# Performance work log

Measured on AMD Instinct MI355X. Metric: run time of the kernel, lower is better.

The kernel has to match this reference:

```python
import jax, jax.numpy as jnp
import numpy as np

ALPHA, BETA, DELTA, TAU, GAMMA = 5.0, 0.6, 0.6, 0.5, 0.5
WINDOW, MOMENTUM = 5, 0.999


def setup_inputs() -> dict:
    key = jax.random.key(0)
    k1, k2 = jax.random.split(key)
    B, C, H, W = 32, 256, 64, 64
    F = jax.random.normal(k1, (B, C, H, W), dtype=jnp.float32)
    S = jnp.eye(C, dtype=jnp.float32)          # EMA similarity buffer (initialized as identity)
    U = jax.random.uniform(k2, (B, C), dtype=jnp.float32)  # replaces torch.bernoulli draw
    return {"F": F, "S": S, "U": U}


def _avg_pool(x, win):
    p = win // 2
    s = jax.lax.reduce_window(x, 0.0, jax.lax.add,
                              (1, 1, win, win), (1, 1, 1, 1),
                              [(0, 0), (0, 0), (p, p), (p, p)])
    return s / (win * win)


def _lrd_mask(F, U):
    # Local Response Density sampling -> boolean mask M [B, C]
    B, C, H, W = F.shape
    a = jax.nn.sigmoid(F.mean(axis=(2, 3)))                     # [B, C]
    max_vals = F.reshape(B, C, -1).max(axis=-1)[:, :, None, None]
    M_bin = (F >= DELTA * max_vals).astype(F.dtype)             # [B, C, H, W]
    density = _avg_pool(M_bin, WINDOW)
    d = (density >= TAU).astype(F.dtype).mean(axis=(2, 3))      # [B, C]
    s = a ** GAMMA * d ** (1.0 - GAMMA)
    s_max = s.max(axis=1, keepdims=True)
    prob = jax.nn.sigmoid(ALPHA * (s - BETA * s_max))
    return U < prob                                             # deterministic bernoulli


def _build_perm(m, S):
    # m: [C] bool selected mask, S: [C, C] similarity -> permutation [C] int32
    C = S.shape[0]
    idx = jnp.arange(C)
    unsel = ~m
    # for each channel, most-similar unselected channel (first max, like torch.argmax)
    masked = jnp.where(unsel[None, :], S, -jnp.inf)
    j = jnp.argmax(masked, axis=1)                              # [C]
    perm = jnp.where(m, j, idx)                                 # perm[selected] = j
    targets = jnp.where(m, j, C)                                # C is out-of-range -> dropped
    perm = perm.at[targets].set(idx, mode='drop')               # perm[j] = selected
    valid = m.any() & unsel.any()
    return jnp.where(valid, perm, idx)


def reference(F, S, U):
    B, C, H, W = F.shape
    # EMA update of channel similarity buffer (no_grad in original)
    F_flat = F.reshape(B, C, -1)
    F_norm = F_flat / (jnp.linalg.norm(F_flat, axis=2, keepdims=True) + 1e-6)
    S_batch = jnp.einsum('bcn,bdn->bcd', F_norm, F_norm).mean(axis=0)
    S_new = jax.lax.stop_gradient(MOMENTUM * S + (1.0 - MOMENTUM) * S_batch)
    # LRD sampling mask and per-sample channel-swap permutation
    M = _lrd_mask(jax.lax.stop_gradient(F), U)                  # [B, C] bool
    perm = jax.vmap(_build_perm, in_axes=(0, None))(M, S_new)   # [B, C]
    # structure-aware channel exchange (gather along channel dim)
    gidx = jnp.broadcast_to(perm[:, :, None, None], (B, C, H, W))
    return jnp.take_along_axis(F, gidx, axis=1)
```

## Files before the change

### kernel.cpp

```cpp
#include <hip/hip_runtime.h>
#include <math.h>

#define BB 32
#define CC 256
#define HH 64
#define WW 64
#define NN 4096

__inline__ __device__ float waveReduceSum(float v) {
    #pragma unroll
    for (int off = 32; off > 0; off >>= 1) v += __shfl_xor(v, off);
    return v;
}
__inline__ __device__ float waveReduceMax(float v) {
    #pragma unroll
    for (int off = 32; off > 0; off >>= 1) v = fmaxf(v, __shfl_xor(v, off));
    return v;
}

__global__ __launch_bounds__(256) void k_prep(const float* __restrict__ F,
                                              float* __restrict__ inv_norm,
                                              float* __restrict__ s_score) {
    const int plane = blockIdx.x;
    const int tid = threadIdx.x;
    __shared__ float bin[4096];
    __shared__ float rowsum[4096];
    __shared__ float swS[4], swQ[4], swM[4];

    const float4* src = (const float4*)(F + (size_t)plane * NN);
    float4 v[4];
    float sum = 0.f, ssq = 0.f, mx = -INFINITY;
    #pragma unroll
    for (int q = 0; q < 4; ++q) {
        v[q] = src[tid + q * 256];
        sum += v[q].x + v[q].y + v[q].z + v[q].w;
        ssq += v[q].x * v[q].x + v[q].y * v[q].y + v[q].z * v[q].z + v[q].w * v[q].w;
        mx = fmaxf(mx, fmaxf(fmaxf(v[q].x, v[q].y), fmaxf(v[q].z, v[q].w)));
    }
    sum = waveReduceSum(sum);
    ssq = waveReduceSum(ssq);
    mx  = waveReduceMax(mx);
    const int w = tid >> 6, ln = tid & 63;
    if (ln == 0) { swS[w] = sum; swQ[w] = ssq; swM[w] = mx; }
    __syncthreads();
    if (tid == 0) {
        swS[0] = swS[0] + swS[1] + swS[2] + swS[3];
        swQ[0] = swQ[0] + swQ[1] + swQ[2] + swQ[3];
        swM[0] = fmaxf(fmaxf(swM[0], swM[1]), fmaxf(swM[2], swM[3]));
    }
    __syncthreads();
    const float totsum = swS[0];
    const float totssq = swQ[0];
    const float thr = 0.6f * swM[0];

    #pragma unroll
    for (int q = 0; q < 4; ++q) {
        const int base = (tid + q * 256) * 4;
        bin[base + 0] = (v[q].x >= thr) ? 1.f : 0.f;
        bin[base + 1] = (v[q].y >= thr) ? 1.f : 0.f;
        bin[base + 2] = (v[q].z >= thr) ? 1.f : 0.f;
        bin[base + 3] = (v[q].w >= thr) ? 1.f : 0.f;
    }
    __syncthreads();

    #pragma unroll
    for (int q = 0; q < 16; ++q) {
        const int p = tid + q * 256;
        const int h = p >> 6, x = p & 63;
        float s5 = 0.f;
        #pragma unroll
        for (int dw = -2; dw <= 2; ++dw) {
            const int xx = x + dw;
            if (xx >= 0 && xx < 64) s5 += bin[h * 64 + xx];
        }
        rowsum[p] = s5;
    }
    __syncthreads();

    int cge = 0;
    #pragma unroll
    for (int q = 0; q < 16; ++q) {
        const int p = tid + q * 256;
        const int h = p >> 6, x = p & 63;
        float cnt = 0.f;
        #pragma unroll
        for (int dh = -2; dh <= 2; ++dh) {
            const int hh = h + dh;
            if (hh >= 0 && hh < 64) cnt += rowsum[hh * 64 + x];
        }
        if (cnt >= 12.5f) cge++;
    }
    float cf = waveReduceSum((float)cge);
    __syncthreads();
    if (ln == 0) swS[w] = cf;
    __syncthreads();
    if (tid == 0) {
        const float total = swS[0] + swS[1] + swS[2] + swS[3];
        const float d = total / 4096.f;
        const float a = 1.f / (1.f + expf(-(totsum / 4096.f)));
        s_score[plane] = sqrtf(a) * sqrtf(d);
        inv_norm[plane] = 1.f / (sqrtf(totssq) + 1e-6f);
    }
}

__global__ __launch_bounds__(256) void k_gram(const float* __restrict__ F,
                                              const float* __restrict__ inv_norm,
                                              float* __restrict__ S_part,
                                              int csh) {
    static const int TI[10] = {0,0,0,0,1,1,1,2,2,3};
    static const int TJ[10] = {0,1,2,3,1,2,3,2,3,3};
    const int t  = blockIdx.x;
    const int bc = blockIdx.y;
    const int b = bc >> csh, chunk = bc & ((1 << csh) - 1);
    const int ti = TI[t], tj = TJ[t];
    const int k0 = chunk << (12 - csh);
    const int iters = 128 >> csh;

    __shared__ float As[32][68];
    __shared__ float Bs[32][68];

    const int tid = threadIdx.x;
    const int lrow = tid >> 2;
    const int kgrp = tid & 3;
    const float* Fb = F + (size_t)b * CC * NN;
    const float scaleA = inv_norm[b * CC + ti * 64 + lrow];
    const float scaleB = inv_norm[b * CC + tj * 64 + lrow];
    const float* gA = Fb + (size_t)(ti * 64 + lrow) * NN + k0 + kgrp * 8;
    const float* gB = Fb + (size_t)(tj * 64 + lrow) * NN + k0 + kgrp * 8;

    const int r0 = (tid >> 4) << 2;
    const int c0 = (tid & 15) << 2;

    float accL2[16];
    #pragma unroll
    for (int e = 0; e < 16; ++e) accL2[e] = 0.f;

    for (int s = 0; s < iters; ++s) {
        const float4 a0 = *(const float4*)(gA);
        const float4 a1 = *(const float4*)(gA + 4);
        const float4 b0 = *(const float4*)(gB);
        const float4 b1 = *(const float4*)(gB + 4);
        __syncthreads();
        const int kb = kgrp * 8;
        As[kb + 0][lrow] = a0.x * scaleA; As[kb + 1][lrow] = a0.y * scaleA;
        As[kb + 2][lrow] = a0.z * scaleA; As[kb + 3][lrow] = a0.w * scaleA;
        As[kb + 4][lrow] = a1.x * scaleA; As[kb + 5][lrow] = a1.y * scaleA;
        As[kb + 6][lrow] = a1.z * scaleA; As[kb + 7][lrow] = a1.w * scaleA;
        Bs[kb + 0][lrow] = b0.x * scaleB; Bs[kb + 1][lrow] = b0.y * scaleB;
        Bs[kb + 2][lrow] = b0.z * scaleB; Bs[kb + 3][lrow] = b0.w * scaleB;
        Bs[kb + 4][lrow] = b1.x * scaleB; Bs[kb + 5][lrow] = b1.y * scaleB;
        Bs[kb + 6][lrow] = b1.z * scaleB; Bs[kb + 7][lrow] = b1.w * scaleB;
        __syncthreads();

        float accL1[16];
        #pragma unroll
        for (int e = 0; e < 16; ++e) accL1[e] = 0.f;
        #pragma unroll
        for (int kk = 0; kk < 32; ++kk) {
            const float4 av = *(const float4*)&As[kk][r0];
            const float4 bv = *(const float4*)&Bs[kk][c0];
            const float ar[4] = {av.x, av.y, av.z, av.w};
            const float br[4] = {bv.x, bv.y, bv.z, bv.w};
            #pragma unroll
            for (int rr = 0; rr < 4; ++rr)
                #pragma unroll
                for (int cc = 0; cc < 4; ++cc)
                    accL1[rr * 4 + cc] += ar[rr] * br[cc];
        }
        #pragma unroll
        for (int e = 0; e < 16; ++e) accL2[e] += accL1[e];
        gA += 32; gB += 32;
    }

    float* dst = S_part + (size_t)(bc * 10 + t) * 4096;
    #pragma unroll
    for (int rr = 0; rr < 4; ++rr)
        #pragma unroll
        for (int cc = 0; cc < 4; ++cc)
            dst[(r0 + rr) * 64 + (c0 + cc)] = accL2[rr * 4 + cc];
}

__global__ __launch_bounds__(256) void k_snew(const float* __restrict__ S_part,
                                              const float* __restrict__ S_old,
                                              float* __restrict__ S_new,
                                              int npart) {
    const int c = blockIdx.x;
    const int d = threadIdx.x;
    if (d < c) return;
    static const int tmap[16] = {0,1,2,3, -1,4,5,6, -1,-1,7,8, -1,-1,-1,9};
    const int t = tmap[((c >> 6) << 2) | (d >> 6)];
    const int r = c & 63, col = d & 63;
    const float* base = S_part + (size_t)t * 4096 + r * 64 + col;
    double sum = 0.0;
    for (int p = 0; p < npart; ++p) sum += (double)base[(size_t)p * 40960];
    const float sb = (float)(sum * (1.0 / 32.0));
    S_new[c * 256 + d] = 0.999f * S_old[c * 256 + d] + 0.001f * sb;
    if (d != c)
        S_new[d * 256 + c] = 0.999f * S_old[d * 256 + c] + 0.001f * sb;
}

__global__ __launch_bounds__(256) void k_perm(const float* __restrict__ s_score,
                                              const float* __restrict__ U,
                                              const float* __restrict__ S_new,
                                              int* __restrict__ perm_g) {
    const int b = blockIdx.x;
    const int c = threadIdx.x;
    __shared__ float red[256];
    __shared__ int m[256];
    __shared__ int jj[256];
    __shared__ int perm[256];

    const float s = s_score[b * 256 + c];
    red[c] = s; __syncthreads();
    for (int off = 128; off > 0; off >>= 1) {
        if (c < off) red[c] = fmaxf(red[c], red[c + off]);
        __syncthreads();
    }
    const float smax = red[0];
    __syncthreads();

    const float prob = 1.f / (1.f + expf(-5.f * (s - 0.6f * smax)));
    const int mi = (U[b * 256 + c] < prob) ? 1 : 0;
    m[c] = mi;
    red[c] = (float)mi;
    __syncthreads();
    for (int off = 128; off > 0; off >>= 1) {
        if (c < off) red[c] += red[c + off];
        __syncthreads();
    }
    const int cnt = (int)red[0];

    float best = -INFINITY; int bj = 0;
    const float* row = S_new + c * 256;
    for (int d2 = 0; d2 < 256; ++d2) {
        const float v = row[d2];
        if (!m[d2] && v > best) { best = v; bj = d2; }
    }
    jj[c] = bj;
    perm[c] = mi ? bj : c;
    __syncthreads();

    const int valid = (cnt > 0) && (cnt < 256);
    if (c == 0 && valid) {
        for (int q = 0; q < 256; ++q)
            if (m[q]) perm[jj[q]] = q;
    }
    __syncthreads();
    perm_g[b * 256 + c] = valid ? perm[c] : c;
}

__global__ __launch_bounds__(256) void k_gather(const float* __restrict__ F,
                                                const int* __restrict__ perm_g,
                                                float* __restrict__ out) {
    const int plane = blockIdx.x;
    const int b = plane >> 8;
    const int p = perm_g[plane];
    const float4* src = (const float4*)(F + ((size_t)b * 256 + p) * NN);
    float4* dst = (float4*)(out + (size_t)plane * NN);
    const int tid = threadIdx.x;
    #pragma unroll
    for (int q = 0; q < 4; ++q) dst[tid + q * 256] = src[tid + q * 256];
}

extern "C" void kernel_launch(void* const* d_in, const int* in_sizes, int n_in,
                              void* d_out, int out_size, void* d_ws, size_t ws_size,
                              hipStream_t stream) {
    const float* F = (const float*)d_in[0];
    const float* S = (const float*)d_in[1];
    const float* U = (const float*)d_in[2];
    float* out = (float*)d_out;

    const size_t need4 = (size_t)128 * 10 * 4096 * 4 + (3 * 8192 + 65536) * 4 + (1 << 16);
    const int csh = (ws_size >= need4) ? 2 : 1;
    const int nch = 1 << csh;
    const int npart = 32 * nch;

    char* ws = (char*)d_ws;
    size_t off = 0;
    float* S_part  = (float*)(ws + off); off += (size_t)npart * 10 * 4096 * 4;
    float* inv_nrm = (float*)(ws + off); off += 8192 * 4;
    float* s_score = (float*)(ws + off); off += 8192 * 4;
    float* S_new   = (float*)(ws + off); off += 65536 * 4;
    int*   perm    = (int*)  (ws + off); off += 8192 * 4;

    k_prep  <<<8192, 256, 0, stream>>>(F, inv_nrm, s_score);
    k_gram  <<<dim3(10, npart), 256, 0, stream>>>(F, inv_nrm, S_part, csh);
    k_snew  <<<256, 256, 0, stream>>>(S_part, S, S_new, npart);
    k_perm  <<<32, 256, 0, stream>>>(s_score, U, S_new, perm);
    k_gather<<<8192, 256, 0, stream>>>(F, perm, out);
}
```

Baseline: 489.2 us.

## Use ballot-based density counting, swizzled gram tiles, and more K-split partitions

The prep kernel now keeps the raw plane in shared memory and computes the 5x5 threshold density with wave ballots and popcounts over bitmasks, replacing the two float shared-memory passes. The gram kernel drops per-element normalization on the shared-memory stores and applies inv_norm at the end. It also XOR-style offsets columns to reduce LDS bank conflicts, uses fmaf accumulation directly, and can split K into 8 chunks when the workspace allows. The EMA reduction uses two accumulators to add ILP. The extra K split raises partial-buffer traffic and reduction work in k_snew.

```diff
diff --git a/kernel.cpp b/kernel.cpp
--- a/kernel.cpp
+++ b/kernel.cpp
@@ -23,8 +23,7 @@
                                               float* __restrict__ s_score) {
     const int plane = blockIdx.x;
     const int tid = threadIdx.x;
-    __shared__ float bin[4096];
-    __shared__ float rowsum[4096];
+    __shared__ float fpl[4096];
     __shared__ float swS[4], swQ[4], swM[4];
 
     const float4* src = (const float4*)(F + (size_t)plane * NN);
@@ -33,6 +32,7 @@
     #pragma unroll
     for (int q = 0; q < 4; ++q) {
         v[q] = src[tid + q * 256];
+        *(float4*)&fpl[(tid + q * 256) * 4] = v[q];
         sum += v[q].x + v[q].y + v[q].z + v[q].w;
         ssq += v[q].x * v[q].x + v[q].y * v[q].y + v[q].z * v[q].z + v[q].w * v[q].w;
         mx = fmaxf(mx, fmaxf(fmaxf(v[q].x, v[q].y), fmaxf(v[q].z, v[q].w)));
@@ -40,8 +40,8 @@
     sum = waveReduceSum(sum);
     ssq = waveReduceSum(ssq);
     mx  = waveReduceMax(mx);
-    const int w = tid >> 6, ln = tid & 63;
-    if (ln == 0) { swS[w] = sum; swQ[w] = ssq; swM[w] = mx; }
+    const int w = tid >> 6, lane = tid & 63;
+    if (lane == 0) { swS[w] = sum; swQ[w] = ssq; swM[w] = mx; }
     __syncthreads();
     if (tid == 0) {
         swS[0] = swS[0] + swS[1] + swS[2] + swS[3];
@@ -52,47 +52,28 @@
     const float totsum = swS[0];
     const float totssq = swQ[0];
     const float thr = 0.6f * swM[0];
-
-    #pragma unroll
-    for (int q = 0; q < 4; ++q) {
-        const int base = (tid + q * 256) * 4;
-        bin[base + 0] = (v[q].x >= thr) ? 1.f : 0.f;
-        bin[base + 1] = (v[q].y >= thr) ? 1.f : 0.f;
-        bin[base + 2] = (v[q].z >= thr) ? 1.f : 0.f;
-        bin[base + 3] = (v[q].w >= thr) ? 1.f : 0.f;
-    }
-    __syncthreads();
-
-    #pragma unroll
-    for (int q = 0; q < 16; ++q) {
-        const int p = tid + q * 256;
-        const int h = p >> 6, x = p & 63;
-        float s5 = 0.f;
-        #pragma unroll
-        for (int dw = -2; dw <= 2; ++dw) {
-            const int xx = x + dw;
-            if (xx >= 0 && xx < 64) s5 += bin[h * 64 + xx];
+    __syncthreads();
+
+    int hh[20];
+    #pragma unroll
+    for (int j = 0; j < 20; ++j) {
+        const int row = 16 * w - 2 + j;
+        unsigned long long m = 0ull;
+        if (row >= 0 && row < 64) {
+            m = __ballot(fpl[row * 64 + lane] >= thr);
         }
-        rowsum[p] = s5;
-    }
-    __syncthreads();
-
+        const unsigned long long sh =
+            (lane >= 2) ? (m >> (lane - 2)) : (m << (2 - lane));
+        hh[j] = (int)__popcll(sh & 31ull);
+    }
     int cge = 0;
     #pragma unroll
-    for (int q = 0; q < 16; ++q) {
-        const int p = tid + q * 256;
-        const int h = p >> 6, x = p & 63;
-        float cnt = 0.f;
-        #pragma unroll
-        for (int dh = -2; dh <= 2; ++dh) {
-            const int hh = h + dh;
-            if (hh >= 0 && hh < 64) cnt += rowsum[hh * 64 + x];
-        }
-        if (cnt >= 12.5f) cge++;
+    for (int r = 0; r < 16; ++r) {
+        const int c5 = hh[r] + hh[r + 1] + hh[r + 2] + hh[r + 3] + hh[r + 4];
+        cge += (c5 >= 13) ? 1 : 0;
     }
     float cf = waveReduceSum((float)cge);
-    __syncthreads();
-    if (ln == 0) swS[w] = cf;
+    if (lane == 0) swS[w] = cf;
     __syncthreads();
     if (tid == 0) {
         const float total = swS[0] + swS[1] + swS[2] + swS[3];
@@ -114,7 +95,7 @@
     const int b = bc >> csh, chunk = bc & ((1 << csh) - 1);
     const int ti = TI[t], tj = TJ[t];
     const int k0 = chunk << (12 - csh);
-    const int iters = 128 >> csh;
+    const int iters = (4096 >> csh) >> 5;
 
     __shared__ float As[32][68];
     __shared__ float Bs[32][68];
@@ -123,17 +104,18 @@
     const int lrow = tid >> 2;
     const int kgrp = tid & 3;
     const float* Fb = F + (size_t)b * CC * NN;
-    const float scaleA = inv_norm[b * CC + ti * 64 + lrow];
-    const float scaleB = inv_norm[b * CC + tj * 64 + lrow];
     const float* gA = Fb + (size_t)(ti * 64 + lrow) * NN + k0 + kgrp * 8;
     const float* gB = Fb + (size_t)(tj * 64 + lrow) * NN + k0 + kgrp * 8;
 
+    const int colW = (lrow + ((kgrp & 1) << 4)) & 63;
+    const int kb = kgrp * 8;
+
     const int r0 = (tid >> 4) << 2;
     const int c0 = (tid & 15) << 2;
 
-    float accL2[16];
-    #pragma unroll
-    for (int e = 0; e < 16; ++e) accL2[e] = 0.f;
+    float acc[16];
+    #pragma unroll
+    for (int e = 0; e < 16; ++e) acc[e] = 0.f;
 
     for (int s = 0; s < iters; ++s) {
         const float4 a0 = *(const float4*)(gA);
@@ -141,43 +123,44 @@
         const float4 b0 = *(const float4*)(gB);
         const float4 b1 = *(const float4*)(gB + 4);
         __syncthreads();
-        const int kb = kgrp * 8;
-        As[kb + 0][lrow] = a0.x * scaleA; As[kb + 1][lrow] = a0.y * scaleA;
-        As[kb + 2][lrow] = a0.z * scaleA; As[kb + 3][lrow] = a0.w * scaleA;
-        As[kb + 4][lrow] = a1.x * scaleA; As[kb + 5][lrow] = a1.y * scaleA;
-        As[kb + 6][lrow] = a1.z * scaleA; As[kb + 7][lrow] = a1.w * scaleA;
-        Bs[kb + 0][lrow] = b0.x * scaleB; Bs[kb + 1][lrow] = b0.y * scaleB;
-        Bs[kb + 2][lrow] = b0.z * scaleB; Bs[kb + 3][lrow] = b0.w * scaleB;
-        Bs[kb + 4][lrow] = b1.x * scaleB; Bs[kb + 5][lrow] = b1.y * scaleB;
-        Bs[kb + 6][lrow] = b1.z * scaleB; Bs[kb + 7][lrow] = b1.w * scaleB;
-        __syncthreads();
-
-        float accL1[16];
-        #pragma unroll
-        for (int e = 0; e < 16; ++e) accL1[e] = 0.f;
+        {
+            const float va[8] = {a0.x,a0.y,a0.z,a0.w,a1.x,a1.y,a1.z,a1.w};
+            const float vb[8] = {b0.x,b0.y,b0.z,b0.w,b1.x,b1.y,b1.z,b1.w};
+            #pragma unroll
+            for (int j = 0; j < 8; ++j) {
+                As[kb + j][colW] = va[j];
+                Bs[kb + j][colW] = vb[j];
+            }
+        }
+        __syncthreads();
+
         #pragma unroll
         for (int kk = 0; kk < 32; ++kk) {
-            const float4 av = *(const float4*)&As[kk][r0];
-            const float4 bv = *(const float4*)&Bs[kk][c0];
+            const int off = ((kk >> 3) & 1) << 4;
+            const float4 av = *(const float4*)&As[kk][(r0 + off) & 63];
+            const float4 bv = *(const float4*)&Bs[kk][(c0 + off) & 63];
             const float ar[4] = {av.x, av.y, av.z, av.w};
             const float br[4] = {bv.x, bv.y, bv.z, bv.w};
             #pragma unroll
             for (int rr = 0; rr < 4; ++rr)
                 #pragma unroll
                 for (int cc = 0; cc < 4; ++cc)
-                    accL1[rr * 4 + cc] += ar[rr] * br[cc];
+                    acc[rr * 4 + cc] = fmaf(ar[rr], br[cc], acc[rr * 4 + cc]);
         }
-        #pragma unroll
-        for (int e = 0; e < 16; ++e) accL2[e] += accL1[e];
         gA += 32; gB += 32;
     }
 
+    const float* invA = inv_norm + b * CC + ti * 64;
+    const float* invB = inv_norm + b * CC + tj * 64;
+    float sA[4], sB[4];
+    #pragma unroll
+    for (int e = 0; e < 4; ++e) { sA[e] = invA[r0 + e]; sB[e] = invB[c0 + e]; }
     float* dst = S_part + (size_t)(bc * 10 + t) * 4096;
     #pragma unroll
     for (int rr = 0; rr < 4; ++rr)
         #pragma unroll
         for (int cc = 0; cc < 4; ++cc)
-            dst[(r0 + rr) * 64 + (c0 + cc)] = accL2[rr * 4 + cc];
+            dst[(r0 + rr) * 64 + (c0 + cc)] = acc[rr * 4 + cc] * sA[rr] * sB[cc];
 }
 
 __global__ __launch_bounds__(256) void k_snew(const float* __restrict__ S_part,
@@ -191,9 +174,14 @@
     const int t = tmap[((c >> 6) << 2) | (d >> 6)];
     const int r = c & 63, col = d & 63;
     const float* base = S_part + (size_t)t * 4096 + r * 64 + col;
-    double sum = 0.0;
-    for (int p = 0; p < npart; ++p) sum += (double)base[(size_t)p * 40960];
-    const float sb = (float)(sum * (1.0 / 32.0));
+    double s0 = 0.0, s1 = 0.0;
+    int p = 0;
+    for (; p + 1 < npart; p += 2) {
+        s0 += (double)base[(size_t)p * 40960];
+        s1 += (double)base[(size_t)(p + 1) * 40960];
+    }
+    for (; p < npart; ++p) s0 += (double)base[(size_t)p * 40960];
+    const float sb = (float)((s0 + s1) * (1.0 / 32.0));
     S_new[c * 256 + d] = 0.999f * S_old[c * 256 + d] + 0.001f * sb;
     if (d != c)
         S_new[d * 256 + c] = 0.999f * S_old[d * 256 + c] + 0.001f * sb;
@@ -270,10 +258,11 @@
     const float* U = (const float*)d_in[2];
     float* out = (float*)d_out;
 
-    const size_t need4 = (size_t)128 * 10 * 4096 * 4 + (3 * 8192 + 65536) * 4 + (1 << 16);
-    const int csh = (ws_size >= need4) ? 2 : 1;
-    const int nch = 1 << csh;
-    const int npart = 32 * nch;
+    const size_t extras = (size_t)(3 * 8192 + 65536) * 4 + 65536;
+    int csh = 1;
+    if (ws_size >= (size_t)(32 << 3) * 10 * 4096 * 4 + extras) csh = 3;
+    else if (ws_size >= (size_t)(32 << 2) * 10 * 4096 * 4 + extras) csh = 2;
+    const int npart = 32 << csh;
 
     char* ws = (char*)d_ws;
     size_t off = 0;
```

Measured after the change: 449.0 us. 1.09x faster.
